# Kernel tuning notes

Measured on AMD Instinct MI355X. Metric: run time of the kernel, lower is better.

Reference implementation:

```python
import jax, jax.numpy as jnp
import numpy as np

M_POW = 4   # m: number of visual-graph powers
N_POW = 4   # n: number of text-graph powers
T = 32      # temporal length, forced by torch.eye(32) in GraphFusion
EPS_BN = 1e-5


def conv1d_same(x, w, b):
    # x: (B, Cin, L), w: (Cout, Cin, 3) -> (B, Cout, L), padding=1
    y = jax.lax.conv_general_dilated(x, w, window_strides=(1,), padding=[(1, 1)],
                                     dimension_numbers=("NCH", "OIH", "NCH"))
    return y + b[None, :, None]


def setup_inputs() -> dict:
    key = jax.random.key(0)
    ks = jax.random.split(key, 10)
    b, c = 128, 5
    d = {}
    d["v_feature"] = jax.random.normal(ks[0], (b, c, T, 2048), jnp.float32)
    d["t_feature"] = jax.random.normal(ks[1], (b, c, T, 768), jnp.float32)
    # Temporal embedding convs (Conv1d k=3, pad=1)
    d["wv"] = jax.random.normal(ks[2], (32, 2048, 3), jnp.float32) * 0.02
    d["bv"] = jnp.zeros((32,), jnp.float32)
    d["wt"] = jax.random.normal(ks[3], (32, 768, 3), jnp.float32) * 0.02
    d["bt"] = jnp.zeros((32,), jnp.float32)
    # GraphFusion learned (m, n) bilinear matrix: torch.normal(0, 1)
    d["fusion_a"] = jax.random.normal(ks[4], (M_POW, N_POW), jnp.float32)
    # NormalHead (BN-WVAD style, in_channel=32, hidden 2 -> 1 -> 1, all k=1 convs)
    d["w1"] = jax.random.normal(ks[5], (2, 32), jnp.float32) * 0.1
    d["b1"] = jnp.zeros((2,), jnp.float32)
    d["g1"] = jnp.ones((2,), jnp.float32)
    d["be1"] = jnp.zeros((2,), jnp.float32)
    d["w2"] = jax.random.normal(ks[6], (1, 2), jnp.float32) * 0.1
    d["b2"] = jnp.zeros((1,), jnp.float32)
    d["g2"] = jnp.ones((1,), jnp.float32)
    d["be2"] = jnp.zeros((1,), jnp.float32)
    d["w3"] = jax.random.normal(ks[7], (1, 1), jnp.float32) * 0.1
    d["b3"] = jnp.zeros((1,), jnp.float32)
    return d


def _forward(v_feature, t_feature, wv, bv, wt, bt, fusion_a,
             w1, b1, g1, be1, w2, b2, g2, be2, w3, b3):
    b, c, t, feat_v = v_feature.shape
    B = b * c
    fv = v_feature.reshape(B, t, feat_v)
    ft = t_feature.reshape(B, t, t_feature.shape[3])
    # Temporal: permute -> conv1d(k=3,pad=1) -> relu -> permute
    fv = jax.nn.relu(conv1d_same(fv.transpose(0, 2, 1), wv, bv)).transpose(0, 2, 1)  # (B,t,32)
    ft = jax.nn.relu(conv1d_same(ft.transpose(0, 2, 1), wt, bt)).transpose(0, 2, 1)  # (B,t,32)

    # GraphFusion
    def l2n(x):
        return x / jnp.maximum(jnp.linalg.norm(x, axis=2, keepdims=True), 1e-12)
    f_v = l2n(fv)
    f_t = l2n(ft)
    a_v = jax.nn.relu(jnp.einsum('bid,bjd->bij', f_v, f_v))  # (B,t,t)
    a_t = jax.nn.relu(jnp.einsum('bid,bjd->bij', f_t, f_t))  # (B,t,t)
    eye = jnp.broadcast_to(jnp.eye(t, dtype=a_v.dtype), (B, t, t))
    # power 0 replaced by identity, as in the torch code
    av_p = jnp.stack([eye] + [a_v ** i for i in range(1, M_POW)], axis=0)  # (m,B,t,t)
    at_p = jnp.stack([eye] + [a_t ** j for j in range(1, N_POW)], axis=0)  # (n,B,t,t)
    # einsum('bijk,kl,blij->bij') with the permutes undone == 'kbij,kl,lbij->bij'
    a_fused = jnp.einsum('kbij,kl,lbij->bij', av_p, fusion_a, at_p)
    a_fused = jax.nn.relu(a_fused)
    a_fused = a_fused / (jnp.max(a_fused) + 0.01)

    # NormalHead on x = a_fused.permute(0,2,1) : (B, C=t, L=t)
    x = a_fused.transpose(0, 2, 1)

    def bn(h, g, beta):  # training-mode BatchNorm1d over (N, L) per channel
        mu = h.mean(axis=(0, 2), keepdims=True)
        var = h.var(axis=(0, 2), keepdims=True)
        return (h - mu) * jax.lax.rsqrt(var + EPS_BN) * g[None, :, None] + beta[None, :, None]

    x1 = jnp.einsum('oc,bcl->bol', w1, x) + b1[None, :, None]
    h1 = jax.nn.relu(bn(x1, g1, be1))
    x2 = jnp.einsum('oc,bcl->bol', w2, h1) + b2[None, :, None]
    h2 = jax.nn.relu(bn(x2, g2, be2))
    scores = jax.nn.sigmoid(jnp.einsum('oc,bcl->bol', w3, h2) + b3[None, :, None])  # (B,1,t)
    normal_scores = scores.reshape(b, c, t).mean(axis=1)  # (b, t), crop-averaged
    return (normal_scores, a_v, a_t, a_fused)


def reference(v_feature, t_feature, wv, bv, wt, bt, fusion_a,
              w1, b1, g1, be1, w2, b2, g2, be2, w3, b3):
    return _forward(v_feature, t_feature, wv, bv, wt, bt, fusion_a,
                    w1, b1, g1, be1, w2, b2, g2, be2, w3, b3)
```

## Files before the change

kernel.cpp:

```cpp
#include <hip/hip_runtime.h>
#include <math.h>


__global__ __launch_bounds__(256) void pack_kernel(
    const float* __restrict__ wv, const float* __restrict__ wt,
    float* __restrict__ wvP, float* __restrict__ wtP,
    float* __restrict__ scal, float* __restrict__ zbuf, int nz) {
    int gid = blockIdx.x * 256 + threadIdx.x;
    if (gid < 16) scal[gid] = 0.f;
    for (int i = gid; i < nz; i += gridDim.x * 256) zbuf[i] = 0.f;
    const int NV = 32 * 2048 * 3;
    const int NT = 32 * 768 * 3;
    if (gid < NV) {
        int o = gid / 6144, rem = gid % 6144;
        int c = rem / 3, k = rem % 3;
        wvP[c * 96 + k * 32 + o] = wv[gid];
    } else if (gid < NV + NT) {
        int s = gid - NV;
        int o = s / 2304, rem = s % 2304;
        int c = rem / 3, k = rem % 3;
        wtP[c * 96 + k * 32 + o] = wt[s];
    }
}

__global__ __launch_bounds__(256, 8) void conv_kernel(
    const float* __restrict__ xv, const float* __restrict__ wvP,
    const float* __restrict__ xt, const float* __restrict__ wtP,
    float* __restrict__ yv, float* __restrict__ yt) {
    int bid = blockIdx.x;
    const float* x; const float* wP; float* y; int Cin;
    if (bid < 1280) { x = xv; wP = wvP; y = yv; Cin = 2048; }
    else { bid -= 1280; x = xt; wP = wtP; y = yt; Cin = 768; }
    int Ch = Cin >> 1;
    int b = bid >> 1, half = bid & 1;
    int c0g = half * Ch;
    int nchunk = Ch >> 5;
    int tid = threadIdx.x, wave = tid >> 6, lane = tid & 63;
    int t0 = (lane >> 3) * 4;
    int o0 = (lane & 7) * 4;
    __shared__ float smem[32 * 36 + 32 * 96];
    float* x_sh = smem;
    float* w_sh = smem + 32 * 36;
    float acc[4][4] = {{0.f}};
    const float* xb = x + (size_t)b * 32 * Cin + c0g;
    const float* wb = wP + (size_t)c0g * 96;
    int ts = tid >> 3, i4 = (tid & 7) * 4;
    for (int ch = 0; ch < nchunk; ++ch) {
        int c0 = ch << 5;
        __syncthreads();
        float4 xq = *(const float4*)(xb + (size_t)ts * Cin + c0 + i4);
        x_sh[(i4 + 0) * 36 + ts + 1] = xq.x;
        x_sh[(i4 + 1) * 36 + ts + 1] = xq.y;
        x_sh[(i4 + 2) * 36 + ts + 1] = xq.z;
        x_sh[(i4 + 3) * 36 + ts + 1] = xq.w;
        if (tid < 32) { x_sh[tid * 36] = 0.f; x_sh[tid * 36 + 33] = 0.f; }
        const float4* wsrc = (const float4*)(wb + (size_t)c0 * 96);
        float4* wdst = (float4*)w_sh;
#pragma unroll
        for (int e = 0; e < 3; ++e) wdst[tid + 256 * e] = wsrc[tid + 256 * e];
        __syncthreads();
        const float* xr = x_sh + (wave * 8) * 36 + t0;
        const float* wr = w_sh + (wave * 8) * 96 + o0;
#pragma unroll
        for (int ci = 0; ci < 8; ++ci) {
            float4 xa = *(const float4*)(xr);
            float2 xc = *(const float2*)(xr + 4);
            float xvv[6] = {xa.x, xa.y, xa.z, xa.w, xc.x, xc.y};
            float4 w0 = *(const float4*)(wr);
            float4 w1 = *(const float4*)(wr + 32);
            float4 w2 = *(const float4*)(wr + 64);
            float wk0[4] = {w0.x, w0.y, w0.z, w0.w};
            float wk1[4] = {w1.x, w1.y, w1.z, w1.w};
            float wk2[4] = {w2.x, w2.y, w2.z, w2.w};
#pragma unroll
            for (int i = 0; i < 4; ++i) {
#pragma unroll
                for (int j = 0; j < 4; ++j) {
                    float a = acc[i][j];
                    a = fmaf(xvv[i],     wk0[j], a);
                    a = fmaf(xvv[i + 1], wk1[j], a);
                    a = fmaf(xvv[i + 2], wk2[j], a);
                    acc[i][j] = a;
                }
            }
            xr += 36; wr += 96;
        }
    }
    __syncthreads();
    float* red = smem;
#pragma unroll
    for (int i = 0; i < 4; ++i)
#pragma unroll
        for (int j = 0; j < 4; ++j)
            red[wave * 1024 + (t0 + i) * 32 + o0 + j] = acc[i][j];
    __syncthreads();
#pragma unroll
    for (int e = 0; e < 4; ++e) {
        int out = tid + 256 * e;
        float s = red[out] + red[1024 + out] + red[2048 + out] + red[3072 + out];
        atomicAdd(&y[(size_t)b * 1024 + out], s);
    }
}

__global__ __launch_bounds__(256) void s2_kernel(
    const float* __restrict__ fvp, const float* __restrict__ ftp,
    const float* __restrict__ bv, const float* __restrict__ bt,
    const float* __restrict__ fuse, float* __restrict__ out_av,
    float* __restrict__ out_at, float* __restrict__ out_af,
    unsigned int* __restrict__ maxslot) {
    int b = blockIdx.x, tid = threadIdx.x;
    __shared__ float Fv[32][33], Ft[32][33], inv[64], wmax[4];
#pragma unroll
    for (int e = 0; e < 4; ++e) {
        int idx = tid + 256 * e;
        int i = idx >> 5, j = idx & 31;
        Fv[i][j] = fmaxf(fvp[b * 1024 + idx] + bv[j], 0.f);
        Ft[i][j] = fmaxf(ftp[b * 1024 + idx] + bt[j], 0.f);
    }
    __syncthreads();
    {
        int row = tid >> 3, cg = (tid & 7) * 4;
        float sv = 0.f, st = 0.f;
#pragma unroll
        for (int q = 0; q < 4; ++q) {
            float v = Fv[row][cg + q]; sv = fmaf(v, v, sv);
            float u = Ft[row][cg + q]; st = fmaf(u, u, st);
        }
        sv += __shfl_xor(sv, 1); sv += __shfl_xor(sv, 2); sv += __shfl_xor(sv, 4);
        st += __shfl_xor(st, 1); st += __shfl_xor(st, 2); st += __shfl_xor(st, 4);
        if ((tid & 7) == 0) {
            inv[row]      = rsqrtf(fmaxf(sv, 1e-24f));
            inv[32 + row] = rsqrtf(fmaxf(st, 1e-24f));
        }
    }
    __syncthreads();
    float fa[16];
#pragma unroll
    for (int q = 0; q < 16; ++q) fa[q] = fuse[q];
    float lmax = 0.f;
#pragma unroll
    for (int e = 0; e < 4; ++e) {
        int idx = tid + 256 * e;
        int i = idx >> 5, j = idx & 31;
        float dv = 0.f, dt_ = 0.f;
        for (int c = 0; c < 32; ++c) {
            dv  = fmaf(Fv[i][c], Fv[j][c], dv);
            dt_ = fmaf(Ft[i][c], Ft[j][c], dt_);
        }
        float av = fmaxf(dv  * inv[i] * inv[j], 0.f);
        float at = fmaxf(dt_ * inv[32 + i] * inv[32 + j], 0.f);
        out_av[b * 1024 + idx] = av;
        out_at[b * 1024 + idx] = at;
        float pv0 = (i == j) ? 1.f : 0.f;
        float pv1 = av, pv2 = av * av, pv3 = pv2 * av;
        float pt1 = at, pt2 = at * at, pt3 = pt2 * at;
        float af = 0.f;
        af += (fa[0] * pv0 + fa[4] * pv1 + fa[8]  * pv2 + fa[12] * pv3) * pv0;
        af += (fa[1] * pv0 + fa[5] * pv1 + fa[9]  * pv2 + fa[13] * pv3) * pt1;
        af += (fa[2] * pv0 + fa[6] * pv1 + fa[10] * pv2 + fa[14] * pv3) * pt2;
        af += (fa[3] * pv0 + fa[7] * pv1 + fa[11] * pv2 + fa[15] * pv3) * pt3;
        float r = fmaxf(af, 0.f);
        out_af[b * 1024 + idx] = r;
        lmax = fmaxf(lmax, r);
    }
    for (int off = 1; off < 64; off <<= 1)
        lmax = fmaxf(lmax, __shfl_xor(lmax, off));
    if ((tid & 63) == 0) wmax[tid >> 6] = lmax;
    __syncthreads();
    if (tid == 0) {
        float m = fmaxf(fmaxf(wmax[0], wmax[1]), fmaxf(wmax[2], wmax[3]));
        atomicMax(maxslot, __float_as_uint(m));
    }
}

__global__ __launch_bounds__(256) void s3_kernel(
    float* __restrict__ af, const float* __restrict__ w1,
    const float* __restrict__ b1, float* __restrict__ x1,
    float* __restrict__ scal) {
    int b = blockIdx.x, tid = threadIdx.x;
    __shared__ float A[32][33];
    float inv = 1.0f / (__uint_as_float(((const unsigned int*)scal)[0]) + 0.01f);
#pragma unroll
    for (int e = 0; e < 4; ++e) {
        int idx = tid + 256 * e;
        float v = af[b * 1024 + idx] * inv;
        af[b * 1024 + idx] = v;
        A[idx >> 5][idx & 31] = v;
    }
    __syncthreads();
    if (tid < 64) {
        int o = tid >> 5, l = tid & 31;
        float s = b1[o];
        for (int c = 0; c < 32; ++c) s = fmaf(w1[o * 32 + c], A[l][c], s);
        x1[(size_t)(b * 2 + o) * 32 + l] = s;
        float s1 = s, s2 = s * s;
        for (int off = 1; off < 32; off <<= 1) {
            s1 += __shfl_xor(s1, off);
            s2 += __shfl_xor(s2, off);
        }
        if (l == 0) {
            atomicAdd(&scal[1 + o], s1);
            atomicAdd(&scal[3 + o], s2);
        }
    }
}

__global__ __launch_bounds__(256) void s4_kernel(
    const float* __restrict__ x1, const float* __restrict__ g1,
    const float* __restrict__ be1, const float* __restrict__ w2,
    const float* __restrict__ b2, float* __restrict__ x2,
    float* __restrict__ scal) {
    int idx = blockIdx.x * 256 + threadIdx.x;
    const float N = 20480.f;
    float mu0 = scal[1] / N, mu1 = scal[2] / N;
    float va0 = scal[3] / N - mu0 * mu0, va1 = scal[4] / N - mu1 * mu1;
    float rs0 = rsqrtf(va0 + 1e-5f), rs1 = rsqrtf(va1 + 1e-5f);
    int b = idx >> 5, l = idx & 31;
    float h0 = fmaxf((x1[(size_t)(b * 2 + 0) * 32 + l] - mu0) * rs0 * g1[0] + be1[0], 0.f);
    float h1 = fmaxf((x1[(size_t)(b * 2 + 1) * 32 + l] - mu1) * rs1 * g1[1] + be1[1], 0.f);
    float v = w2[0] * h0 + w2[1] * h1 + b2[0];
    x2[idx] = v;
    float s1 = v, s2 = v * v;
    for (int off = 1; off < 64; off <<= 1) {
        s1 += __shfl_xor(s1, off);
        s2 += __shfl_xor(s2, off);
    }
    __shared__ float ps[4][2];
    int lane = threadIdx.x & 63, w = threadIdx.x >> 6;
    if (lane == 0) { ps[w][0] = s1; ps[w][1] = s2; }
    __syncthreads();
    if (threadIdx.x == 0) {
        atomicAdd(&scal[5], ps[0][0] + ps[1][0] + ps[2][0] + ps[3][0]);
        atomicAdd(&scal[6], ps[0][1] + ps[1][1] + ps[2][1] + ps[3][1]);
    }
}

__global__ __launch_bounds__(256) void s5_kernel(
    const float* __restrict__ x2, const float* __restrict__ g2,
    const float* __restrict__ be2, const float* __restrict__ w3,
    const float* __restrict__ b3, float* __restrict__ ns,
    const float* __restrict__ scal) {
    int idx = blockIdx.x * 256 + threadIdx.x;
    const float N = 20480.f;
    float mu = scal[5] / N;
    float var = scal[6] / N - mu * mu;
    float rs = rsqrtf(var + 1e-5f);
    int bb = idx >> 5, t = idx & 31;
    float s = 0.f;
#pragma unroll
    for (int crop = 0; crop < 5; ++crop) {
        int b = bb * 5 + crop;
        float h = fmaxf((x2[b * 32 + t] - mu) * rs * g2[0] + be2[0], 0.f);
        float z = w3[0] * h + b3[0];
        s += 1.f / (1.f + expf(-z));
    }
    ns[idx] = s * 0.2f;
}

extern "C" void kernel_launch(void* const* d_in, const int* in_sizes, int n_in,
                              void* d_out, int out_size, void* d_ws, size_t ws_size,
                              hipStream_t stream) {
    const float* v_feat = (const float*)d_in[0];
    const float* t_feat = (const float*)d_in[1];
    const float* wv  = (const float*)d_in[2];
    const float* bv  = (const float*)d_in[3];
    const float* wt  = (const float*)d_in[4];
    const float* bt  = (const float*)d_in[5];
    const float* fuse= (const float*)d_in[6];
    const float* w1  = (const float*)d_in[7];
    const float* b1  = (const float*)d_in[8];
    const float* g1  = (const float*)d_in[9];
    const float* be1 = (const float*)d_in[10];
    const float* w2  = (const float*)d_in[11];
    const float* b2  = (const float*)d_in[12];
    const float* g2  = (const float*)d_in[13];
    const float* be2 = (const float*)d_in[14];
    const float* w3  = (const float*)d_in[15];
    const float* b3  = (const float*)d_in[16];

    float* ws   = (float*)d_ws;
    float* scal = ws;
    float* wvP  = ws + 16;
    float* wtP  = wvP + 196608;
    float* fv   = wtP + 73728;
    float* ft   = fv + 655360;
    float* x1   = ft + 655360;
    float* x2   = x1 + 40960;

    float* out_ns = (float*)d_out;
    float* out_av = out_ns + 4096;
    float* out_at = out_av + 655360;
    float* out_af = out_at + 655360;

    pack_kernel<<<1056, 256, 0, stream>>>(wv, wt, wvP, wtP, scal, fv, 2 * 655360);
    conv_kernel<<<2560, 256, 0, stream>>>(v_feat, wvP, t_feat, wtP, fv, ft);
    s2_kernel<<<640, 256, 0, stream>>>(fv, ft, bv, bt, fuse, out_av, out_at,
                                       out_af, (unsigned int*)scal);
    s3_kernel<<<640, 256, 0, stream>>>(out_af, w1, b1, x1, scal);
    s4_kernel<<<80, 256, 0, stream>>>(x1, g1, be1, w2, b2, x2, scal);
    s5_kernel<<<16, 256, 0, stream>>>(x2, g2, be2, w3, b3, out_ns, scal);
}
```

Measured before the change: 424.4 us.

## Use split-bf16 MFMA for temporal convolutions, one block per sample

Replaces the FP32 FMA conv kernel with a matrix-core kernel. Inputs and weights are split into bf16 hi/lo pairs and combined with three MFMA products per step to approximate fp32 precision. Each block now computes one whole sample for both the visual and text convs, which removes the channel-split atomics and the zeroing of the output buffers. Weights are prepacked into the MFMA fragment layout and read straight from global memory. The costs are extra conversion work when staging x into LDS and fewer, longer blocks (640 instead of 2560).

```diff
diff --git a/kernel.cpp b/kernel.cpp
--- a/kernel.cpp
+++ b/kernel.cpp
@@ -1,105 +1,138 @@
 #include <hip/hip_runtime.h>
+#include <hip/hip_bf16.h>
 #include <math.h>
 
+
+typedef __attribute__((ext_vector_type(8))) short short8;
+typedef __attribute__((ext_vector_type(4))) float f32x4;
+
+#define XROW 132
+
+__device__ __forceinline__ unsigned short f2bf(float f) {
+    __hip_bfloat16 h = __float2bfloat16(f);
+    return *reinterpret_cast<unsigned short*>(&h);
+}
+__device__ __forceinline__ float bf2f(unsigned short u) {
+    return __uint_as_float(((unsigned int)u) << 16);
+}
+__device__ __forceinline__ short8 lds_frag(const unsigned short* p) {
+    union { uint2 u2[2]; short8 s; } r;
+    r.u2[0] = *reinterpret_cast<const uint2*>(p);
+    r.u2[1] = *reinterpret_cast<const uint2*>(p + 4);
+    return r.s;
+}
+__device__ __forceinline__ short8 glb_frag(const unsigned short* p) {
+    union { uint4 u; short8 s; } r;
+    r.u = *reinterpret_cast<const uint4*>(p);
+    return r.s;
+}
 
 __global__ __launch_bounds__(256) void pack_kernel(
     const float* __restrict__ wv, const float* __restrict__ wt,
-    float* __restrict__ wvP, float* __restrict__ wtP,
-    float* __restrict__ scal, float* __restrict__ zbuf, int nz) {
+    unsigned short* __restrict__ wvpk, unsigned short* __restrict__ wtpk,
+    float* __restrict__ scal) {
     int gid = blockIdx.x * 256 + threadIdx.x;
     if (gid < 16) scal[gid] = 0.f;
-    for (int i = gid; i < nz; i += gridDim.x * 256) zbuf[i] = 0.f;
-    const int NV = 32 * 2048 * 3;
-    const int NT = 32 * 768 * 3;
+    const int NV = 196608, NT = 73728;
     if (gid < NV) {
         int o = gid / 6144, rem = gid % 6144;
         int c = rem / 3, k = rem % 3;
-        wvP[c * 96 + k * 32 + o] = wv[gid];
+        int s = c >> 5, cp = c & 31;
+        float f = wv[gid];
+        unsigned short h = f2bf(f);
+        unsigned short l = f2bf(f - bf2f(h));
+        int base = (s * 3 + k) * 2048 + o * 32 + cp;
+        wvpk[base] = h;
+        wvpk[base + 1024] = l;
     } else if (gid < NV + NT) {
-        int s = gid - NV;
-        int o = s / 2304, rem = s % 2304;
+        int g = gid - NV;
+        int o = g / 2304, rem = g % 2304;
         int c = rem / 3, k = rem % 3;
-        wtP[c * 96 + k * 32 + o] = wt[s];
-    }
-}
-
-__global__ __launch_bounds__(256, 8) void conv_kernel(
-    const float* __restrict__ xv, const float* __restrict__ wvP,
-    const float* __restrict__ xt, const float* __restrict__ wtP,
+        int s = c >> 5, cp = c & 31;
+        float f = wt[g];
+        unsigned short h = f2bf(f);
+        unsigned short l = f2bf(f - bf2f(h));
+        int base = (s * 3 + k) * 2048 + o * 32 + cp;
+        wtpk[base] = h;
+        wtpk[base + 1024] = l;
+    }
+}
+
+__device__ __forceinline__ void conv_phase(
+    const float* __restrict__ xb, int Cin,
+    const unsigned short* __restrict__ wpk,
+    unsigned short* hiT, unsigned short* loT,
+    float* __restrict__ yout, int tid, int wave, int lane) {
+    __syncthreads();
+    if (tid < XROW) {
+        hiT[tid] = 0; hiT[33 * XROW + tid] = 0;
+        loT[tid] = 0; loT[33 * XROW + tid] = 0;
+    }
+    f32x4 acc0 = {0.f, 0.f, 0.f, 0.f};
+    f32x4 acc1 = {0.f, 0.f, 0.f, 0.f};
+    int tm = wave & 1, tn = wave >> 1;
+    int m = lane & 15, quad = lane >> 4;
+    int c4 = tid & 31, tg = tid >> 5;
+    int nchunk = Cin >> 7;
+    for (int ch = 0; ch < nchunk; ++ch) {
+        int c0 = ch << 7;
+        __syncthreads();
+#pragma unroll
+        for (int pass = 0; pass < 4; ++pass) {
+            int t = tg + (pass << 3);
+            const float4 xq = *reinterpret_cast<const float4*>(
+                xb + (size_t)t * Cin + c0 + (c4 << 2));
+            unsigned short h0 = f2bf(xq.x), h1 = f2bf(xq.y);
+            unsigned short h2 = f2bf(xq.z), h3 = f2bf(xq.w);
+            unsigned short l0 = f2bf(xq.x - bf2f(h0));
+            unsigned short l1 = f2bf(xq.y - bf2f(h1));
+            unsigned short l2 = f2bf(xq.z - bf2f(h2));
+            unsigned short l3 = f2bf(xq.w - bf2f(h3));
+            int widx = (t + 1) * XROW + (c4 << 2);
+            *reinterpret_cast<uint2*>(hiT + widx) =
+                make_uint2(h0 | ((unsigned int)h1 << 16), h2 | ((unsigned int)h3 << 16));
+            *reinterpret_cast<uint2*>(loT + widx) =
+                make_uint2(l0 | ((unsigned int)l1 << 16), l2 | ((unsigned int)l3 << 16));
+        }
+        __syncthreads();
+        int sbase = c0 >> 5;
+        int arow0 = (tm << 4) + m;
+        int bofs = ((tn << 4) + m) * 32 + (quad << 3);
+#pragma unroll
+        for (int sl = 0; sl < 4; ++sl) {
+            int acol = (sl << 5) + (quad << 3);
+            const unsigned short* bbase = wpk + (size_t)(sbase + sl) * 6144 + bofs;
+#pragma unroll
+            for (int k = 0; k < 3; ++k) {
+                short8 Ah = lds_frag(hiT + (arow0 + k) * XROW + acol);
+                short8 Al = lds_frag(loT + (arow0 + k) * XROW + acol);
+                short8 Bh = glb_frag(bbase + k * 2048);
+                short8 Bl = glb_frag(bbase + k * 2048 + 1024);
+                acc0 = __builtin_amdgcn_mfma_f32_16x16x32_bf16(Ah, Bh, acc0, 0, 0, 0);
+                acc1 = __builtin_amdgcn_mfma_f32_16x16x32_bf16(Ah, Bl, acc1, 0, 0, 0);
+                acc1 = __builtin_amdgcn_mfma_f32_16x16x32_bf16(Al, Bh, acc1, 0, 0, 0);
+            }
+        }
+    }
+    int ocol = (tn << 4) + m;
+#pragma unroll
+    for (int r = 0; r < 4; ++r) {
+        int t = (tm << 4) + (quad << 2) + r;
+        yout[t * 32 + ocol] = acc0[r] + acc1[r];
+    }
+}
+
+__global__ __launch_bounds__(256, 4) void conv_mfma_kernel(
+    const float* __restrict__ xv, const unsigned short* __restrict__ wvpk,
+    const float* __restrict__ xt, const unsigned short* __restrict__ wtpk,
     float* __restrict__ yv, float* __restrict__ yt) {
-    int bid = blockIdx.x;
-    const float* x; const float* wP; float* y; int Cin;
-    if (bid < 1280) { x = xv; wP = wvP; y = yv; Cin = 2048; }
-    else { bid -= 1280; x = xt; wP = wtP; y = yt; Cin = 768; }
-    int Ch = Cin >> 1;
-    int b = bid >> 1, half = bid & 1;
-    int c0g = half * Ch;
-    int nchunk = Ch >> 5;
-    int tid = threadIdx.x, wave = tid >> 6, lane = tid & 63;
-    int t0 = (lane >> 3) * 4;
-    int o0 = (lane & 7) * 4;
-    __shared__ float smem[32 * 36 + 32 * 96];
-    float* x_sh = smem;
-    float* w_sh = smem + 32 * 36;
-    float acc[4][4] = {{0.f}};
-    const float* xb = x + (size_t)b * 32 * Cin + c0g;
-    const float* wb = wP + (size_t)c0g * 96;
-    int ts = tid >> 3, i4 = (tid & 7) * 4;
-    for (int ch = 0; ch < nchunk; ++ch) {
-        int c0 = ch << 5;
-        __syncthreads();
-        float4 xq = *(const float4*)(xb + (size_t)ts * Cin + c0 + i4);
-        x_sh[(i4 + 0) * 36 + ts + 1] = xq.x;
-        x_sh[(i4 + 1) * 36 + ts + 1] = xq.y;
-        x_sh[(i4 + 2) * 36 + ts + 1] = xq.z;
-        x_sh[(i4 + 3) * 36 + ts + 1] = xq.w;
-        if (tid < 32) { x_sh[tid * 36] = 0.f; x_sh[tid * 36 + 33] = 0.f; }
-        const float4* wsrc = (const float4*)(wb + (size_t)c0 * 96);
-        float4* wdst = (float4*)w_sh;
-#pragma unroll
-        for (int e = 0; e < 3; ++e) wdst[tid + 256 * e] = wsrc[tid + 256 * e];
-        __syncthreads();
-        const float* xr = x_sh + (wave * 8) * 36 + t0;
-        const float* wr = w_sh + (wave * 8) * 96 + o0;
-#pragma unroll
-        for (int ci = 0; ci < 8; ++ci) {
-            float4 xa = *(const float4*)(xr);
-            float2 xc = *(const float2*)(xr + 4);
-            float xvv[6] = {xa.x, xa.y, xa.z, xa.w, xc.x, xc.y};
-            float4 w0 = *(const float4*)(wr);
-            float4 w1 = *(const float4*)(wr + 32);
-            float4 w2 = *(const float4*)(wr + 64);
-            float wk0[4] = {w0.x, w0.y, w0.z, w0.w};
-            float wk1[4] = {w1.x, w1.y, w1.z, w1.w};
-            float wk2[4] = {w2.x, w2.y, w2.z, w2.w};
-#pragma unroll
-            for (int i = 0; i < 4; ++i) {
-#pragma unroll
-                for (int j = 0; j < 4; ++j) {
-                    float a = acc[i][j];
-                    a = fmaf(xvv[i],     wk0[j], a);
-                    a = fmaf(xvv[i + 1], wk1[j], a);
-                    a = fmaf(xvv[i + 2], wk2[j], a);
-                    acc[i][j] = a;
-                }
-            }
-            xr += 36; wr += 96;
-        }
-    }
-    __syncthreads();
-    float* red = smem;
-#pragma unroll
-    for (int i = 0; i < 4; ++i)
-#pragma unroll
-        for (int j = 0; j < 4; ++j)
-            red[wave * 1024 + (t0 + i) * 32 + o0 + j] = acc[i][j];
-    __syncthreads();
-#pragma unroll
-    for (int e = 0; e < 4; ++e) {
-        int out = tid + 256 * e;
-        float s = red[out] + red[1024 + out] + red[2048 + out] + red[3072 + out];
-        atomicAdd(&y[(size_t)b * 1024 + out], s);
-    }
+    __shared__ unsigned short hiT[34 * XROW], loT[34 * XROW];
+    int b = blockIdx.x, tid = threadIdx.x;
+    int wave = tid >> 6, lane = tid & 63;
+    conv_phase(xv + (size_t)b * 32 * 2048, 2048, wvpk, hiT, loT,
+               yv + (size_t)b * 1024, tid, wave, lane);
+    conv_phase(xt + (size_t)b * 32 * 768, 768, wtpk, hiT, loT,
+               yt + (size_t)b * 1024, tid, wave, lane);
 }
 
 __global__ __launch_bounds__(256) void s2_kernel(
@@ -168,8 +201,8 @@
     if ((tid & 63) == 0) wmax[tid >> 6] = lmax;
     __syncthreads();
     if (tid == 0) {
-        float m = fmaxf(fmaxf(wmax[0], wmax[1]), fmaxf(wmax[2], wmax[3]));
-        atomicMax(maxslot, __float_as_uint(m));
+        float mx = fmaxf(fmaxf(wmax[0], wmax[1]), fmaxf(wmax[2], wmax[3]));
+        atomicMax(maxslot, __float_as_uint(mx));
     }
 }
 
@@ -280,9 +313,9 @@
 
     float* ws   = (float*)d_ws;
     float* scal = ws;
-    float* wvP  = ws + 16;
-    float* wtP  = wvP + 196608;
-    float* fv   = wtP + 73728;
+    unsigned short* wvpk = (unsigned short*)(ws + 16);
+    unsigned short* wtpk = (unsigned short*)(ws + 16 + 196608);
+    float* fv   = ws + 16 + 196608 + 73728;
     float* ft   = fv + 655360;
     float* x1   = ft + 655360;
     float* x2   = x1 + 40960;
@@ -292,8 +325,8 @@
     float* out_at = out_av + 655360;
     float* out_af = out_at + 655360;
 
-    pack_kernel<<<1056, 256, 0, stream>>>(wv, wt, wvP, wtP, scal, fv, 2 * 655360);
-    conv_kernel<<<2560, 256, 0, stream>>>(v_feat, wvP, t_feat, wtP, fv, ft);
+    pack_kernel<<<1056, 256, 0, stream>>>(wv, wt, wvpk, wtpk, scal);
+    conv_mfma_kernel<<<640, 256, 0, stream>>>(v_feat, wvpk, t_feat, wtpk, fv, ft);
     s2_kernel<<<640, 256, 0, stream>>>(fv, ft, bv, bt, fuse, out_av, out_at,
                                        out_af, (unsigned int*)scal);
     s3_kernel<<<640, 256, 0, stream>>>(out_af, w1, b1, x1, scal);
```

After: 396.4 us. 6.6% less time.
